# Optimization experiments

Hardware: AMD Instinct MI355X
Metric: run time of the kernel (lower is better)

The kernel has to match this reference:

```python
import jax, jax.numpy as jnp
import numpy as np

TEMPERATURE = 0.5
EPS = 1e-12  # matches torch F.normalize default eps


def setup_inputs() -> dict:
    key = jax.random.key(0)
    k1, k2 = jax.random.split(key)
    B, D = 4096, 1024
    emb_i = jax.random.normal(k1, (B, D), dtype=jnp.float32)
    emb_j = jax.random.normal(k2, (B, D), dtype=jnp.float32)
    return {"emb_i": emb_i, "emb_j": emb_j}


def _l2_normalize(x):
    # torch F.normalize(dim=1): x / max(||x||, eps)
    n = jnp.sqrt(jnp.sum(x * x, axis=1, keepdims=True))
    return x / jnp.maximum(n, EPS)


def reference(emb_i, emb_j):
    B = emb_i.shape[0]
    z_i = _l2_normalize(emb_i)
    z_j = _l2_normalize(emb_j)
    z = jnp.concatenate([z_i, z_j], axis=0)  # [2B, D]
    # cosine similarity of unit vectors == dot product -> single GEMM
    sim = jnp.einsum('nd,md->nm', z, z)  # [2B, 2B]
    sim_ij = jnp.diagonal(sim, offset=B)   # [B]
    sim_ji = jnp.diagonal(sim, offset=-B)  # [B]
    positives = jnp.concatenate([sim_ij, sim_ji], axis=0)  # [2B]
    nominator = jnp.exp(positives / TEMPERATURE)
    neg_mask = 1.0 - jnp.eye(2 * B, dtype=sim.dtype)
    denominator = jnp.sum(neg_mask * jnp.exp(sim / TEMPERATURE), axis=1)  # [2B]
    loss_partial = -jnp.log(nominator / denominator)
    return jnp.sum(loss_partial) / (2 * B)
```

## Files before the change

kernel.cpp:

```cpp
#include <hip/hip_runtime.h>
#include <hip/hip_bf16.h>
#include <math.h>

#define B_ROWS 4096
#define N_ROWS 8192
#define D_DIM  1024
#define NTILES 64
#define NSLOT  64
#define NPAIRS (NTILES * (NTILES + 1) / 2)
#define NXCD 8

#define BM 128
#define BK 64
#define NT (D_DIM / BK)
#define SLOT_BYTES 16384
#define RING 2

typedef __attribute__((ext_vector_type(4))) int i32x4;

__device__ __forceinline__ void load_lds_16B(const void* g, void* l) {
  __builtin_amdgcn_global_load_lds(
      (const __attribute__((address_space(1))) void*)g,
      (__attribute__((address_space(3))) void*)l, 16, 0, 0);
}

#define VMCNT0() asm volatile("s_waitcnt vmcnt(0)" ::: "memory")
#define LGKM0()  asm volatile("s_waitcnt lgkmcnt(0)" ::: "memory")
#define BARRIER() asm volatile("s_barrier" ::: "memory")

__global__ void normalize_kernel(const float* __restrict__ emb_i,
                                 const float* __restrict__ emb_j,
                                 char* __restrict__ zq,
                                 float* __restrict__ rowS,
                                 float* __restrict__ dn) {
  const int row = blockIdx.x;
  const int tid = threadIdx.x;
  const float* src = (row < B_ROWS) ? (emb_i + (size_t)row * D_DIM)
                                    : (emb_j + (size_t)(row - B_ROWS) * D_DIM);
  float4 v = reinterpret_cast<const float4*>(src)[tid];
  float ss = v.x * v.x + v.y * v.y + v.z * v.z + v.w * v.w;
#pragma unroll
  for (int m = 32; m; m >>= 1) ss += __shfl_xor(ss, m, 64);
  __shared__ float red[4];
  const int wave = tid >> 6, lane = tid & 63;
  if (lane == 0) red[wave] = ss;
  __syncthreads();
  const float tot = red[0] + red[1] + red[2] + red[3];
  const float scale = 1.0f / fmaxf(sqrtf(tot), 1e-12f);

  const float z0 = v.x * scale, z1 = v.y * scale, z2 = v.z * scale,
              z3 = v.w * scale;
  float am = fmaxf(fmaxf(fabsf(z0), fabsf(z1)), fmaxf(fabsf(z2), fabsf(z3)));
#pragma unroll
  for (int m = 32; m; m >>= 1) am = fmaxf(am, __shfl_xor(am, m, 64));
  __syncthreads();
  if (lane == 0) red[wave] = am;
  __syncthreads();
  const float zmax =
      fmaxf(fmaxf(red[0], red[1]), fmaxf(red[2], red[3]));
  const float s = zmax * (1.0f / 127.0f);
  const float inv = (zmax > 0.0f) ? 127.0f / zmax : 0.0f;

  const int q0 = (int)rintf(z0 * inv), q1 = (int)rintf(z1 * inv);
  const int q2 = (int)rintf(z2 * inv), q3 = (int)rintf(z3 * inv);
  char4 pk;
  pk.x = (char)q0;
  pk.y = (char)q1;
  pk.z = (char)q2;
  pk.w = (char)q3;
  reinterpret_cast<char4*>(zq)[(size_t)row * (D_DIM / 4) + tid] = pk;

  float ds = (float)(q0 * q0 + q1 * q1 + q2 * q2 + q3 * q3);
#pragma unroll
  for (int m = 32; m; m >>= 1) ds += __shfl_xor(ds, m, 64);
  __syncthreads();
  if (lane == 0) red[wave] = ds;
  __syncthreads();
  if (tid == 0) {
    dn[row] = s * s * (red[0] + red[1] + red[2] + red[3]);
    rowS[row] = s;
  }
}

__global__ void pos_kernel(const char* __restrict__ zq,
                           const float* __restrict__ rowS,
                           float* __restrict__ pos) {
  const int n = blockIdx.x;
  const int tid = threadIdx.x;
  char4 a = reinterpret_cast<const char4*>(zq + (size_t)n * D_DIM)[tid];
  char4 b =
      reinterpret_cast<const char4*>(zq + (size_t)(n + B_ROWS) * D_DIM)[tid];
  float sdot = (float)((int)a.x * b.x + (int)a.y * b.y + (int)a.z * b.z +
                       (int)a.w * b.w);
#pragma unroll
  for (int m = 32; m; m >>= 1) sdot += __shfl_xor(sdot, m, 64);
  __shared__ float red[4];
  const int wave = tid >> 6, lane = tid & 63;
  if (lane == 0) red[wave] = sdot;
  __syncthreads();
  if (tid == 0)
    pos[n] = rowS[n] * rowS[n + B_ROWS] * (red[0] + red[1] + red[2] + red[3]);
}

__global__ __launch_bounds__(256, 4) void simexp_kernel(
    const char* __restrict__ zq, const float* __restrict__ rowS,
    float* __restrict__ partial) {
  __shared__ __align__(16) char ldsbuf[RING * SLOT_BYTES];
  __shared__ float rowAcc[BM];
  __shared__ float colAcc[BM];
  __shared__ float sRow[BM];
  __shared__ float sCol[BM];

  const int tid = threadIdx.x;

  const int work = (blockIdx.x % NXCD) * (NPAIRS / NXCD) + blockIdx.x / NXCD;

  int rem = work;
  int ti = 0;
  while (rem >= NTILES - ti) {
    rem -= NTILES - ti;
    ++ti;
  }
  const int tj = ti + rem;
  const bool diag = (ti == tj);
  const int row0 = ti * BM;
  const int m0 = tj * BM;

  if (tid < BM) {
    rowAcc[tid] = 0.0f;
    sRow[tid] = rowS[row0 + tid];
  } else {
    colAcc[tid - BM] = 0.0f;
    sCol[tid - BM] = rowS[m0 + tid - BM];
  }

  const int wave = tid >> 6, lane = tid & 63;
  const int wr = wave >> 1, wc = wave & 1;
  const int l15 = lane & 15, l4 = lane >> 4;

  const int rs = tid >> 2;
  const int qs = tid & 3;
  const int ss = qs ^ ((rs >> 1) & 3);
  const char* gA0 = zq + (size_t)(row0 + rs) * D_DIM + ss * 16;
  const size_t dR64 = (size_t)64 * D_DIM;
  const size_t dB = (size_t)(m0 - row0) * D_DIM;
  const int WA0 = tid * 16;
  const int WA1 = tid * 16 + 4096;

  int offA[4], offB[4];
#pragma unroll
  for (int mi = 0; mi < 4; ++mi) {
    const int rA = wr * 64 + mi * 16 + l15;
    offA[mi] = rA * 64 + ((l4 ^ ((rA >> 1) & 3)) << 4);
    const int rB = wc * 64 + mi * 16 + l15;
    offB[mi] = 8192 + rB * 64 + ((l4 ^ ((rB >> 1) & 3)) << 4);
  }

  i32x4 acc[4][4];
#pragma unroll
  for (int mi = 0; mi < 4; ++mi)
#pragma unroll
    for (int ni = 0; ni < 4; ++ni) acc[mi][ni] = (i32x4){0, 0, 0, 0};

#define STAGE(kk)                                                      \
  {                                                                    \
    char* slot_ = ldsbuf + ((kk) & (RING - 1)) * SLOT_BYTES;           \
    const char* g_ = gA0 + (size_t)(kk)*BK;                            \
    load_lds_16B(g_, slot_ + WA0);                                     \
    load_lds_16B(g_ + dR64, slot_ + WA1);                              \
    load_lds_16B(g_ + dB, slot_ + 8192 + WA0);                         \
    load_lds_16B(g_ + dB + dR64, slot_ + 8192 + WA1);                  \
  }

#define COMPUTE(kk)                                                    \
  {                                                                    \
    const char* slot_ = ldsbuf + ((kk) & (RING - 1)) * SLOT_BYTES;     \
    i32x4 af[4], bf[4];                                                \
    _Pragma("unroll") for (int mi = 0; mi < 4; ++mi)                   \
        af[mi] = *reinterpret_cast<const i32x4*>(slot_ + offA[mi]);    \
    _Pragma("unroll") for (int ni = 0; ni < 4; ++ni)                   \
        bf[ni] = *reinterpret_cast<const i32x4*>(slot_ + offB[ni]);    \
    __builtin_amdgcn_s_setprio(1);                                     \
    _Pragma("unroll") for (int mi = 0; mi < 4; ++mi)                   \
        _Pragma("unroll") for (int ni = 0; ni < 4; ++ni) acc[mi][ni] = \
            __builtin_amdgcn_mfma_i32_16x16x64_i8(af[mi], bf[ni],      \
                                                  acc[mi][ni], 0, 0,   \
                                                  0);                  \
    __builtin_amdgcn_s_setprio(0);                                     \
  }

  STAGE(0);
  VMCNT0();
  BARRIER();

  for (int k = 0; k < NT - 1; ++k) {
    STAGE(k + 1);
    COMPUTE(k);
    VMCNT0();
    BARRIER();
  }
  COMPUTE(NT - 1);

  const float C2 = 2.8853900817779268f;
  float cCol0 = C2 * sCol[wc * 64 + 0 * 16 + l15];
  float cCol1 = C2 * sCol[wc * 64 + 1 * 16 + l15];
  float cCol2 = C2 * sCol[wc * 64 + 2 * 16 + l15];
  float cCol3 = C2 * sCol[wc * 64 + 3 * 16 + l15];

#pragma unroll
  for (int mi = 0; mi < 4; ++mi) {
#pragma unroll
    for (int j = 0; j < 4; ++j) {
      const float srow = sRow[wr * 64 + mi * 16 + l4 * 4 + j];
      acc[mi][0][j] = __float_as_int(exp2f(cCol0 * srow * (float)acc[mi][0][j]));
      acc[mi][1][j] = __float_as_int(exp2f(cCol1 * srow * (float)acc[mi][1][j]));
      acc[mi][2][j] = __float_as_int(exp2f(cCol2 * srow * (float)acc[mi][2][j]));
      acc[mi][3][j] = __float_as_int(exp2f(cCol3 * srow * (float)acc[mi][3][j]));
    }
  }

#pragma unroll
  for (int mi = 0; mi < 4; ++mi) {
#pragma unroll
    for (int j = 0; j < 4; ++j) {
      float s = __int_as_float(acc[mi][0][j]) + __int_as_float(acc[mi][1][j]) +
                __int_as_float(acc[mi][2][j]) + __int_as_float(acc[mi][3][j]);
      s += __shfl_xor(s, 1, 64);
      s += __shfl_xor(s, 2, 64);
      s += __shfl_xor(s, 4, 64);
      s += __shfl_xor(s, 8, 64);
      if (l15 == 0) atomicAdd(&rowAcc[wr * 64 + mi * 16 + l4 * 4 + j], s);
    }
  }

  if (!diag) {
#pragma unroll
    for (int ni = 0; ni < 4; ++ni) {
      float s = 0.0f;
#pragma unroll
      for (int mi = 0; mi < 4; ++mi)
#pragma unroll
        for (int j = 0; j < 4; ++j) s += __int_as_float(acc[mi][ni][j]);
      s += __shfl_xor(s, 16, 64);
      s += __shfl_xor(s, 32, 64);
      if (l4 == 0) atomicAdd(&colAcc[wc * 64 + ni * 16 + l15], s);
    }
  }

  LGKM0();
  BARRIER();
  if (tid < BM) partial[(size_t)(row0 + tid) * NSLOT + tj] = rowAcc[tid];
  if (!diag && tid >= BM && tid < 2 * BM)
    partial[(size_t)(m0 + tid - BM) * NSLOT + ti] = colAcc[tid - BM];
#undef STAGE
#undef COMPUTE
}

__global__ void rowloss_kernel(const float* __restrict__ partial,
                               const float* __restrict__ dn,
                               const float* __restrict__ pos,
                               float* __restrict__ blockSum) {
  const int tid = threadIdx.x;
  const int n = blockIdx.x * 256 + tid;
  const float C2 = 2.8853900817779268f;
  float S = 0.0f;
#pragma unroll
  for (int c = 0; c < NSLOT; ++c) S += partial[(size_t)n * NSLOT + c];
  const float den = S - exp2f(dn[n] * C2);
  const float p = pos[(n < B_ROWS) ? n : (n - B_ROWS)];
  float acc = -2.0f * p + logf(den);
#pragma unroll
  for (int m = 32; m; m >>= 1) acc += __shfl_xor(acc, m, 64);
  __shared__ float red[4];
  const int wave = tid >> 6, lane = tid & 63;
  if (lane == 0) red[wave] = acc;
  __syncthreads();
  if (tid == 0) blockSum[blockIdx.x] = red[0] + red[1] + red[2] + red[3];
}

__global__ void final2_kernel(const float* __restrict__ blockSum,
                              float* __restrict__ out) {
  const int tid = threadIdx.x;
  float v = (tid < 32) ? blockSum[tid] : 0.0f;
#pragma unroll
  for (int m = 32; m; m >>= 1) v += __shfl_xor(v, m, 64);
  if (tid == 0) out[0] = v / (float)N_ROWS;
}

extern "C" void kernel_launch(void* const* d_in, const int* in_sizes, int n_in,
                              void* d_out, int out_size, void* d_ws,
                              size_t ws_size, hipStream_t stream) {
  const float* emb_i = (const float*)d_in[0];
  const float* emb_j = (const float*)d_in[1];
  float* out = (float*)d_out;

  char* zq = (char*)d_ws;
  char* p = (char*)d_ws + (size_t)N_ROWS * D_DIM;
  float* partial = (float*)p;
  p += (size_t)N_ROWS * NSLOT * sizeof(float);
  float* dn = (float*)p;
  p += (size_t)N_ROWS * sizeof(float);
  float* rowS = (float*)p;
  p += (size_t)N_ROWS * sizeof(float);
  float* pos = (float*)p;
  p += (size_t)B_ROWS * sizeof(float);
  float* blockSum = (float*)p;

  normalize_kernel<<<N_ROWS, 256, 0, stream>>>(emb_i, emb_j, zq, rowS, dn);
  pos_kernel<<<B_ROWS, 256, 0, stream>>>(zq, rowS, pos);
  simexp_kernel<<<NPAIRS, 256, 0, stream>>>(zq, rowS, partial);
  rowloss_kernel<<<N_ROWS / 256, 256, 0, stream>>>(partial, dn, pos, blockSum);
  final2_kernel<<<1, 64, 0, stream>>>(blockSum, out);
}
```

Before: 82.17 us.

## Fold diagonal and positive-pair dots into GEMM tiles, drop pos kernel

The normalize kernel now handles one row per wave with no LDS or block barriers, and it no longer computes the quantized self-dot. The separate pos_kernel is removed. The self-similarity (dn) and positive-pair similarity (pos) are instead read straight from the int8 MFMA accumulators of the diagonal tiles and of the tiles offset by 32 in the simexp kernel. This saves one kernel launch and one pass over the quantized matrix, at the cost of a small conditional epilogue in the GEMM kernel.

```diff
diff --git a/kernel.cpp b/kernel.cpp
--- a/kernel.cpp
+++ b/kernel.cpp
@@ -28,83 +28,59 @@
 #define LGKM0()  asm volatile("s_waitcnt lgkmcnt(0)" ::: "memory")
 #define BARRIER() asm volatile("s_barrier" ::: "memory")
 
-__global__ void normalize_kernel(const float* __restrict__ emb_i,
-                                 const float* __restrict__ emb_j,
-                                 char* __restrict__ zq,
-                                 float* __restrict__ rowS,
-                                 float* __restrict__ dn) {
-  const int row = blockIdx.x;
-  const int tid = threadIdx.x;
+__global__ __launch_bounds__(256) void normalize_kernel(
+    const float* __restrict__ emb_i, const float* __restrict__ emb_j,
+    char* __restrict__ zq, float* __restrict__ rowS) {
+  const int lane = threadIdx.x & 63;
+  const int wave = threadIdx.x >> 6;
+  const int row = blockIdx.x * 4 + wave;
   const float* src = (row < B_ROWS) ? (emb_i + (size_t)row * D_DIM)
                                     : (emb_j + (size_t)(row - B_ROWS) * D_DIM);
-  float4 v = reinterpret_cast<const float4*>(src)[tid];
-  float ss = v.x * v.x + v.y * v.y + v.z * v.z + v.w * v.w;
+  const float4* s4 = reinterpret_cast<const float4*>(src);
+  float4 v0 = s4[lane], v1 = s4[lane + 64], v2 = s4[lane + 128],
+         v3 = s4[lane + 192];
+
+  float ss = v0.x * v0.x + v0.y * v0.y + v0.z * v0.z + v0.w * v0.w +
+             v1.x * v1.x + v1.y * v1.y + v1.z * v1.z + v1.w * v1.w +
+             v2.x * v2.x + v2.y * v2.y + v2.z * v2.z + v2.w * v2.w +
+             v3.x * v3.x + v3.y * v3.y + v3.z * v3.z + v3.w * v3.w;
 #pragma unroll
   for (int m = 32; m; m >>= 1) ss += __shfl_xor(ss, m, 64);
-  __shared__ float red[4];
-  const int wave = tid >> 6, lane = tid & 63;
-  if (lane == 0) red[wave] = ss;
-  __syncthreads();
-  const float tot = red[0] + red[1] + red[2] + red[3];
-  const float scale = 1.0f / fmaxf(sqrtf(tot), 1e-12f);
-
-  const float z0 = v.x * scale, z1 = v.y * scale, z2 = v.z * scale,
-              z3 = v.w * scale;
-  float am = fmaxf(fmaxf(fabsf(z0), fabsf(z1)), fmaxf(fabsf(z2), fabsf(z3)));
+  const float scale = 1.0f / fmaxf(sqrtf(ss), 1e-12f);
+
+  float z[16];
+  z[0] = v0.x * scale;  z[1] = v0.y * scale;  z[2] = v0.z * scale;
+  z[3] = v0.w * scale;  z[4] = v1.x * scale;  z[5] = v1.y * scale;
+  z[6] = v1.z * scale;  z[7] = v1.w * scale;  z[8] = v2.x * scale;
+  z[9] = v2.y * scale;  z[10] = v2.z * scale; z[11] = v2.w * scale;
+  z[12] = v3.x * scale; z[13] = v3.y * scale; z[14] = v3.z * scale;
+  z[15] = v3.w * scale;
+
+  float am = 0.0f;
+#pragma unroll
+  for (int i = 0; i < 16; ++i) am = fmaxf(am, fabsf(z[i]));
 #pragma unroll
   for (int m = 32; m; m >>= 1) am = fmaxf(am, __shfl_xor(am, m, 64));
-  __syncthreads();
-  if (lane == 0) red[wave] = am;
-  __syncthreads();
-  const float zmax =
-      fmaxf(fmaxf(red[0], red[1]), fmaxf(red[2], red[3]));
-  const float s = zmax * (1.0f / 127.0f);
-  const float inv = (zmax > 0.0f) ? 127.0f / zmax : 0.0f;
-
-  const int q0 = (int)rintf(z0 * inv), q1 = (int)rintf(z1 * inv);
-  const int q2 = (int)rintf(z2 * inv), q3 = (int)rintf(z3 * inv);
-  char4 pk;
-  pk.x = (char)q0;
-  pk.y = (char)q1;
-  pk.z = (char)q2;
-  pk.w = (char)q3;
-  reinterpret_cast<char4*>(zq)[(size_t)row * (D_DIM / 4) + tid] = pk;
-
-  float ds = (float)(q0 * q0 + q1 * q1 + q2 * q2 + q3 * q3);
-#pragma unroll
-  for (int m = 32; m; m >>= 1) ds += __shfl_xor(ds, m, 64);
-  __syncthreads();
-  if (lane == 0) red[wave] = ds;
-  __syncthreads();
-  if (tid == 0) {
-    dn[row] = s * s * (red[0] + red[1] + red[2] + red[3]);
-    rowS[row] = s;
-  }
-}
-
-__global__ void pos_kernel(const char* __restrict__ zq,
-                           const float* __restrict__ rowS,
-                           float* __restrict__ pos) {
-  const int n = blockIdx.x;
-  const int tid = threadIdx.x;
-  char4 a = reinterpret_cast<const char4*>(zq + (size_t)n * D_DIM)[tid];
-  char4 b =
-      reinterpret_cast<const char4*>(zq + (size_t)(n + B_ROWS) * D_DIM)[tid];
-  float sdot = (float)((int)a.x * b.x + (int)a.y * b.y + (int)a.z * b.z +
-                       (int)a.w * b.w);
-#pragma unroll
-  for (int m = 32; m; m >>= 1) sdot += __shfl_xor(sdot, m, 64);
-  __shared__ float red[4];
-  const int wave = tid >> 6, lane = tid & 63;
-  if (lane == 0) red[wave] = sdot;
-  __syncthreads();
-  if (tid == 0)
-    pos[n] = rowS[n] * rowS[n + B_ROWS] * (red[0] + red[1] + red[2] + red[3]);
+  const float s = am * (1.0f / 127.0f);
+  const float inv = (am > 0.0f) ? 127.0f / am : 0.0f;
+
+  char4* dst = reinterpret_cast<char4*>(zq + (size_t)row * D_DIM);
+#pragma unroll
+  for (int i = 0; i < 4; ++i) {
+    char4 pk;
+    pk.x = (char)(int)rintf(z[i * 4 + 0] * inv);
+    pk.y = (char)(int)rintf(z[i * 4 + 1] * inv);
+    pk.z = (char)(int)rintf(z[i * 4 + 2] * inv);
+    pk.w = (char)(int)rintf(z[i * 4 + 3] * inv);
+    dst[lane + 64 * i] = pk;
+  }
+  if (lane == 0) rowS[row] = s;
 }
 
 __global__ __launch_bounds__(256, 4) void simexp_kernel(
     const char* __restrict__ zq, const float* __restrict__ rowS,
-    float* __restrict__ partial) {
+    float* __restrict__ partial, float* __restrict__ dn,
+    float* __restrict__ pos) {
   __shared__ __align__(16) char ldsbuf[RING * SLOT_BYTES];
   __shared__ float rowAcc[BM];
   __shared__ float colAcc[BM];
@@ -201,6 +177,23 @@
   }
   COMPUTE(NT - 1);
 
+  if (diag || tj == ti + 32) {
+    float* dst = diag ? dn : pos;
+    if (wr == wc) {
+#pragma unroll
+      for (int mi = 0; mi < 4; ++mi) {
+#pragma unroll
+        for (int j = 0; j < 4; ++j) {
+          if (l15 == l4 * 4 + j) {
+            const int rloc = wr * 64 + mi * 16 + l4 * 4 + j;
+            dst[row0 + rloc] =
+                sRow[rloc] * sCol[rloc] * (float)acc[mi][mi][j];
+          }
+        }
+      }
+    }
+  }
+
   const float C2 = 2.8853900817779268f;
   float cCol0 = C2 * sCol[wc * 64 + 0 * 16 + l15];
   float cCol1 = C2 * sCol[wc * 64 + 1 * 16 + l15];
@@ -306,9 +299,8 @@
   p += (size_t)B_ROWS * sizeof(float);
   float* blockSum = (float*)p;
 
-  normalize_kernel<<<N_ROWS, 256, 0, stream>>>(emb_i, emb_j, zq, rowS, dn);
-  pos_kernel<<<B_ROWS, 256, 0, stream>>>(zq, rowS, pos);
-  simexp_kernel<<<NPAIRS, 256, 0, stream>>>(zq, rowS, partial);
+  normalize_kernel<<<N_ROWS / 4, 256, 0, stream>>>(emb_i, emb_j, zq, rowS);
+  simexp_kernel<<<NPAIRS, 256, 0, stream>>>(zq, rowS, partial, dn, pos);
   rowloss_kernel<<<N_ROWS / 256, 256, 0, stream>>>(partial, dn, pos, blockSum);
   final2_kernel<<<1, 64, 0, stream>>>(blockSum, out);
 }
```

Measured after the change: 75.89 us, median of 2. 7.6% less time.
